# Kernel optimization log

Hardware: AMD Instinct MI355X
Metric: run time of the kernel (lower is better)

Reference implementation:

```python
import jax, jax.numpy as jnp
import numpy as np

N_NODES = 100000
N_EDGES = 1600000
N_GRAPHS = 128
IN_DIM, HID, OUT_DIM, DOC_DIM = 64, 128, 32, 768
LAYERS = 3


def setup_inputs() -> dict:
    key = jax.random.key(0)
    ks = jax.random.split(key, 24)
    s = 0.05
    inp = {
        "x": jax.random.normal(ks[0], (N_NODES, IN_DIM), jnp.float32),
        "doc_features": jax.random.normal(ks[1], (N_GRAPHS, DOC_DIM), jnp.float32),
        "edge_index": jax.random.randint(ks[2], (2, N_EDGES), 0, N_NODES, jnp.int64),
        "batch": jnp.sort(jax.random.randint(ks[3], (N_NODES,), 0, N_GRAPHS, jnp.int64)),
        # parameters (stored as [in, out] so y = x @ W + b)
        "node_w": jax.random.normal(ks[4], (IN_DIM, HID), jnp.float32) * s,
        "node_b": jnp.zeros((HID,), jnp.float32),
        "ggnn_w": jax.random.normal(ks[5], (LAYERS, HID, HID), jnp.float32) * s,
        "gru_w_ih": jax.random.normal(ks[6], (HID, 3 * HID), jnp.float32) * s,
        "gru_b_ih": jnp.zeros((3 * HID,), jnp.float32),
        "gru_w_hh": jax.random.normal(ks[7], (HID, 3 * HID), jnp.float32) * s,
        "gru_b_hh": jnp.zeros((3 * HID,), jnp.float32),
        "doc_w": jax.random.normal(ks[8], (DOC_DIM, HID), jnp.float32) * s,
        "doc_b": jnp.zeros((HID,), jnp.float32),
        "ln_g": jnp.ones((2 * HID,), jnp.float32),
        "ln_b": jnp.zeros((2 * HID,), jnp.float32),
        "fus_w": jax.random.normal(ks[9], (2 * HID, HID), jnp.float32) * s,
        "fus_b": jnp.zeros((HID,), jnp.float32),
        "task_w": jax.random.normal(ks[10], (HID, OUT_DIM), jnp.float32) * s,
        "task_b": jnp.zeros((OUT_DIM,), jnp.float32),
        "time_w": jax.random.normal(ks[11], (HID, 1), jnp.float32) * s,
        "time_b": jnp.zeros((1,), jnp.float32),
    }
    return inp


def _gru(m, h, w_ih, b_ih, w_hh, b_hh):
    gi = m @ w_ih + b_ih  # [N, 3H]
    gh = h @ w_hh + b_hh
    ir, iz, in_ = jnp.split(gi, 3, axis=-1)
    hr, hz, hn = jnp.split(gh, 3, axis=-1)
    r = jax.nn.sigmoid(ir + hr)
    z = jax.nn.sigmoid(iz + hz)
    n = jnp.tanh(in_ + r * hn)
    return (1.0 - z) * n + z * h


def reference(x, doc_features, node_w, node_b, ggnn_w, gru_w_ih, gru_b_ih,
              gru_w_hh, gru_b_hh, doc_w, doc_b, ln_g, ln_b, fus_w, fus_b,
              task_w, task_b, time_w, time_b, edge_index, batch):
    N = x.shape[0]
    src, dst = edge_index[0], edge_index[1]
    # node projection + ReLU
    h = jax.nn.relu(x @ node_w + node_b)  # [N, H]
    # GatedGraphConv: 3 layers of (linear -> scatter-add over edges -> GRU)
    for i in range(LAYERS):
        m = h @ ggnn_w[i]                              # [N, H]
        agg = jax.ops.segment_sum(m[src], dst, num_segments=N)  # scatter-add
        h = _gru(agg, h, gru_w_ih, gru_b_ih, gru_w_hh, gru_b_hh)
    # global mean pool over graphs
    sums = jax.ops.segment_sum(h, batch, num_segments=N_GRAPHS)  # [G, H]
    cnt = jax.ops.segment_sum(jnp.ones((N,), h.dtype), batch, num_segments=N_GRAPHS)
    pooled = sums / jnp.maximum(cnt, 1.0)[:, None]
    # doc projection + fusion head
    doc_emb = jax.nn.relu(doc_features @ doc_w + doc_b)  # [G, H]
    fusion = jnp.concatenate([pooled, doc_emb], axis=1)  # [G, 2H]
    mu = jnp.mean(fusion, axis=-1, keepdims=True)
    var = jnp.mean(jnp.square(fusion - mu), axis=-1, keepdims=True)
    fusion = (fusion - mu) * jax.lax.rsqrt(var + 1e-5) * ln_g + ln_b
    fusion = jax.nn.relu(fusion @ fus_w + fus_b)  # dropout is identity (eval)
    task_output = fusion @ task_w + task_b
    time_output = fusion @ time_w + time_b
    return (task_output, time_output)
```

## Files before the change

### kernel.cpp

```cpp
#include <hip/hip_runtime.h>

#define N_NODES  100000
#define N_EDGES  1600000
#define N_GRAPHS 128

#define BSH      8
#define BNODES   (1 << BSH)
#define NBUCK    391
#define NBLK_P1  512
#define EPB      (N_EDGES / NBLK_P1)
#define BKT_SCAN_N   (NBUCK * NBLK_P1)
#define SCAN_BLK_BKT 196
#define SCAN_BLK_NODE 98

typedef unsigned short u16;
typedef unsigned int   u32;
typedef __attribute__((ext_vector_type(8))) short short8;
typedef __attribute__((ext_vector_type(4))) float f32x4;

__device__ __forceinline__ float bf2f(u16 v) {
  union { u32 i; float f; } u; u.i = ((u32)v) << 16; return u.f;
}
__device__ __forceinline__ u16 f2bf(float f) {
  union { float f; u32 i; } u; u.f = f;
  u32 r = (u.i + 0x7fffu + ((u.i >> 16) & 1u)) >> 16;
  return (u16)r;
}
__device__ __forceinline__ float sigmoid_f(float x) { return 1.f / (1.f + __expf(-x)); }
__device__ __forceinline__ float tanh_f(float x) {
  x = fminf(15.f, fmaxf(-15.f, x));
  float e = __expf(2.f * x);
  return (e - 1.f) / (e + 1.f);
}
__device__ __forceinline__ int geti(const int* __restrict__ p, int i, int is64) {
  return p[is64 ? (2 * i) : i];
}

__global__ void detect_i64_kernel(const int* __restrict__ ei, const int* __restrict__ batch,
                                  int* __restrict__ flags) {
  int lane = threadIdx.x;
  {
    long long q = (long long)lane * (3200000 / 2 - 1) / 63;
    int pos = (int)(2 * q + 1);
    unsigned long long m = __ballot(ei[pos] != 0);
    if (lane == 0) flags[0] = (m == 0ull) ? 1 : 0;
  }
  {
    long long q = (long long)lane * (100000 / 2 - 1) / 63;
    int pos = (int)(2 * q + 1);
    unsigned long long m = __ballot(batch[pos] != 0);
    if (lane == 0) flags[1] = (m == 0ull) ? 1 : 0;
  }
}


__global__ __launch_bounds__(256)
void bucket_hist(const int* __restrict__ ei, const int* __restrict__ flags,
                 int* __restrict__ bcounts) {
  __shared__ int h[NBUCK];
  const int f = flags[0];
  for (int b = threadIdx.x; b < NBUCK; b += 256) h[b] = 0;
  __syncthreads();
  const int e0 = blockIdx.x * EPB;
  for (int i = threadIdx.x; i < EPB; i += 256) {
    int d = geti(ei, N_EDGES + e0 + i, f);
    atomicAdd(&h[d >> BSH], 1);
  }
  __syncthreads();
  for (int b = threadIdx.x; b < NBUCK; b += 256)
    bcounts[b * NBLK_P1 + blockIdx.x] = h[b];
}

__global__ __launch_bounds__(256)
void bucket_scatter(const int* __restrict__ ei, const int* __restrict__ flags,
                    const int* __restrict__ bbases, u32* __restrict__ bedges) {
  __shared__ int cur[NBUCK];
  const int f = flags[0];
  for (int b = threadIdx.x; b < NBUCK; b += 256)
    cur[b] = bbases[b * NBLK_P1 + blockIdx.x];
  __syncthreads();
  const int e0 = blockIdx.x * EPB;
  for (int i = threadIdx.x; i < EPB; i += 256) {
    int e = e0 + i;
    int d = geti(ei, N_EDGES + e, f);
    int s = geti(ei, e, f);
    int pos = atomicAdd(&cur[d >> BSH], 1);
    bedges[pos] = ((u32)(d & (BNODES - 1)) << 17) | (u32)s;
  }
}

__global__ __launch_bounds__(256)
void node_count(const u32* __restrict__ bedges, const int* __restrict__ bbases,
                int* __restrict__ counts) {
  __shared__ int h[BNODES];
  const int b = blockIdx.x;
  for (int i = threadIdx.x; i < BNODES; i += 256) h[i] = 0;
  __syncthreads();
  const int beg = bbases[b * NBLK_P1];
  const int end = (b + 1 < NBUCK) ? bbases[(b + 1) * NBLK_P1] : N_EDGES;
  for (int e = beg + threadIdx.x; e < end; e += 256)
    atomicAdd(&h[bedges[e] >> 17], 1);
  __syncthreads();
  const int node0 = b << BSH;
  for (int i = threadIdx.x; i < BNODES; i += 256)
    if (node0 + i < N_NODES) counts[node0 + i] = h[i];
}

__global__ __launch_bounds__(256)
void final_scatter(const u32* __restrict__ bedges, const int* __restrict__ bbases,
                   const int* __restrict__ offs, int* __restrict__ ssrc) {
  __shared__ int cur[BNODES];
  const int b = blockIdx.x;
  const int node0 = b << BSH;
  for (int i = threadIdx.x; i < BNODES; i += 256)
    cur[i] = (node0 + i < N_NODES) ? offs[node0 + i] : 0;
  __syncthreads();
  const int beg = bbases[b * NBLK_P1];
  const int end = (b + 1 < NBUCK) ? bbases[(b + 1) * NBLK_P1] : N_EDGES;
  for (int e = beg + threadIdx.x; e < end; e += 256) {
    u32 v = bedges[e];
    int pos = atomicAdd(&cur[v >> 17], 1);
    ssrc[pos] = (int)(v & 0x1FFFFu);
  }
}

__global__ __launch_bounds__(1024)
void scanA_kernel(const int* __restrict__ counts, int n, int* __restrict__ blocksums) {
  __shared__ int red[16];
  int i = blockIdx.x * 1024 + threadIdx.x;
  int v = (i < n) ? counts[i] : 0;
  for (int o = 32; o > 0; o >>= 1) v += __shfl_down(v, o, 64);
  int wv = threadIdx.x >> 6, lane = threadIdx.x & 63;
  if (lane == 0) red[wv] = v;
  __syncthreads();
  if (threadIdx.x < 16) {
    int s = red[threadIdx.x];
    for (int o = 8; o > 0; o >>= 1) s += __shfl_down(s, o, 64);
    if (threadIdx.x == 0) blocksums[blockIdx.x] = s;
  }
}

__global__ void scanB_kernel(const int* __restrict__ blocksums, int nblocks,
                             int* __restrict__ blockbase, int* __restrict__ total_out) {
  if (threadIdx.x == 0) {
    int run = 0;
    for (int b = 0; b < nblocks; ++b) { blockbase[b] = run; run += blocksums[b]; }
    if (total_out) *total_out = run;
  }
}

__global__ __launch_bounds__(1024)
void scanC_kernel(const int* __restrict__ counts, int n, const int* __restrict__ blockbase,
                  int* __restrict__ offsets) {
  __shared__ int buf[1024];
  int t = threadIdx.x;
  int i = blockIdx.x * 1024 + t;
  int v = (i < n) ? counts[i] : 0;
  buf[t] = v;
  __syncthreads();
  for (int o = 1; o < 1024; o <<= 1) {
    int add = (t >= o) ? buf[t - o] : 0;
    __syncthreads();
    buf[t] += add;
    __syncthreads();
  }
  if (i < n) offsets[i] = buf[t] - v + blockbase[blockIdx.x];
}

__global__ void transpose_kernel(const float* __restrict__ in, u16* __restrict__ out, int K, int N) {
  int i = blockIdx.x * 256 + threadIdx.x;
  if (i < K * N) {
    int k = i / N, n = i % N;
    out[n * K + k] = f2bf(in[i]);
  }
}

__global__ void wprime_kernel(const float* __restrict__ ggnn_w, const float* __restrict__ w_ih,
                              float* __restrict__ wp) {
  int i = blockIdx.x * 256 + threadIdx.x;
  if (i >= 3 * 128 * 384) return;
  int l = i / (128 * 384), r = i % (128 * 384), k = r / 384, c = r % 384;
  const float* W = ggnn_w + l * 128 * 128;
  float s = 0.f;
  for (int j = 0; j < 128; ++j) s += W[k * 128 + j] * w_ih[j * 384 + c];
  wp[i] = s;
}

__global__ void build_b2p_kernel(const float* __restrict__ wp, const float* __restrict__ w_hh,
                                 u16* __restrict__ b2p) {
  int g = blockIdx.x * 256 + threadIdx.x;
  if (g >= 8 * 1536 * 8) return;
  int e = g & 7;
  int grp = g >> 3;
  int ci = grp / 1536;
  int idx = grp % 1536;
  int n_lin = idx % 384;
  int ko = idx / 384;
  int k = ci * 32 + ko * 8 + e;
  float v = (k < 128) ? wp[k * 384 + n_lin] : w_hh[(k - 128) * 384 + n_lin];
  b2p[g] = f2bf(v);
}

__global__ __launch_bounds__(256)
void nodeproj_gemm(const float* __restrict__ A, const u16* __restrict__ BT,
                   const float* __restrict__ bias, u16* __restrict__ out, int M)
{
  constexpr int K_DIM = 64, N_DIM = 128, NT = 8, NCHUNK = 2;
  __shared__ u16 B_lds[N_DIM * 40];
  const int tid = threadIdx.x, lane = tid & 63, w = tid >> 6;
  const int strip = blockIdx.x * 64;
  const int ksub = (lane >> 4) * 8;
  union Frag { uint4 u; short8 s; };
  Frag af[NCHUNK];
  const int m_node = strip + w * 16 + (lane & 15);
  const bool avalid = (m_node < M);
#pragma unroll
  for (int ci = 0; ci < NCHUNK; ++ci) {
    int k0 = ci * 32 + ksub;
    short8 sv = {0,0,0,0,0,0,0,0};
    if (avalid) {
      const float* p = A + (size_t)m_node * K_DIM + k0;
      float4 f0 = *(const float4*)p;
      float4 f1 = *(const float4*)(p + 4);
      sv[0]=(short)f2bf(f0.x); sv[1]=(short)f2bf(f0.y); sv[2]=(short)f2bf(f0.z); sv[3]=(short)f2bf(f0.w);
      sv[4]=(short)f2bf(f1.x); sv[5]=(short)f2bf(f1.y); sv[6]=(short)f2bf(f1.z); sv[7]=(short)f2bf(f1.w);
    }
    af[ci].s = sv;
  }
  f32x4 acc[NT];
#pragma unroll
  for (int t = 0; t < NT; ++t) acc[t] = {0.f, 0.f, 0.f, 0.f};
  const int boff = (lane & 15) * 40 + ksub;
#pragma unroll
  for (int ci = 0; ci < NCHUNK; ++ci) {
    if (ci) __syncthreads();
    for (int g = tid; g < N_DIM * 4; g += 256) {
      int n = g >> 2, ko = g & 3;
      uint4 bv = *(const uint4*)(BT + (size_t)n * K_DIM + ci * 32 + ko * 8);
      *(uint4*)(&B_lds[n * 40 + ko * 8]) = bv;
    }
    __syncthreads();
    short8 a = af[ci].s;
#pragma unroll
    for (int t = 0; t < NT; ++t) {
      const short8 b = *(const short8*)(&B_lds[t * 16 * 40 + boff]);
      acc[t] = __builtin_amdgcn_mfma_f32_16x16x32_bf16(a, b, acc[t], 0, 0, 0);
    }
  }
  const int mrow = (lane >> 4) * 4;
#pragma unroll
  for (int t = 0; t < NT; ++t) {
    int col = t * 16 + (lane & 15);
    float bv = bias[col];
#pragma unroll
    for (int r = 0; r < 4; ++r) {
      int node = strip + w * 16 + mrow + r;
      if (node < M) out[(size_t)node * N_DIM + col] = f2bf(fmaxf(acc[t][r] + bv, 0.f));
    }
  }
}

__global__ __launch_bounds__(256)
void gru_gemm(const u16* __restrict__ agg, const u16* __restrict__ h,
              const u16* __restrict__ b2p, const float* __restrict__ b_ih,
              const float* __restrict__ b_hh, u16* __restrict__ hout, int M)
{
  const int tid  = threadIdx.x;
  const int lane = tid & 63;
  const int qc   = tid >> 6;
  const int strip = blockIdx.x * 32;
  const int lrow  = lane & 15;
  const int quad  = lane >> 4;
  const int ksub  = quad * 8;
  if (strip >= M) return;

  f32x4 ar[2][2], az[2][2], ain[2][2], ahn[2][2];
#pragma unroll
  for (int s = 0; s < 2; ++s)
#pragma unroll
    for (int t = 0; t < 2; ++t) {
      ar[s][t] = {0.f,0.f,0.f,0.f}; az[s][t] = {0.f,0.f,0.f,0.f};
      ain[s][t] = {0.f,0.f,0.f,0.f}; ahn[s][t] = {0.f,0.f,0.f,0.f};
    }

  union Frag { uint4 u; short8 s8; };
  const int node0 = strip + lrow;
  const int node1 = strip + 16 + lrow;
  const u16* bb = b2p + ((size_t)quad * 384 + qc * 32 + lrow) * 8;

  Frag a0[2], a1[2], fbr[2][2], fbz[2][2], fbg[2][2];

  auto ldchunk = [&](int ci, int p) {
    const u16* ap = (ci < 4) ? (agg + ci * 32 + ksub) : (h + (ci - 4) * 32 + ksub);
    a0[p].u = *(const uint4*)(ap + (size_t)node0 * 128);
    a1[p].u = *(const uint4*)(ap + (size_t)node1 * 128);
    const u16* cb = bb + ci * 12288;
    fbr[p][0].u = *(const uint4*)(cb);
    fbr[p][1].u = *(const uint4*)(cb + 128);
    fbz[p][0].u = *(const uint4*)(cb + 1024);
    fbz[p][1].u = *(const uint4*)(cb + 1024 + 128);
    fbg[p][0].u = *(const uint4*)(cb + 2048);
    fbg[p][1].u = *(const uint4*)(cb + 2048 + 128);
  };

  ldchunk(0, 0);
#pragma unroll
  for (int ci = 0; ci < 8; ++ci) {
    const int p = ci & 1, q = p ^ 1;
    if (ci < 7) ldchunk(ci + 1, q);
#pragma unroll
    for (int t = 0; t < 2; ++t) {
      ar[0][t] = __builtin_amdgcn_mfma_f32_16x16x32_bf16(a0[p].s8, fbr[p][t].s8, ar[0][t], 0, 0, 0);
      ar[1][t] = __builtin_amdgcn_mfma_f32_16x16x32_bf16(a1[p].s8, fbr[p][t].s8, ar[1][t], 0, 0, 0);
      az[0][t] = __builtin_amdgcn_mfma_f32_16x16x32_bf16(a0[p].s8, fbz[p][t].s8, az[0][t], 0, 0, 0);
      az[1][t] = __builtin_amdgcn_mfma_f32_16x16x32_bf16(a1[p].s8, fbz[p][t].s8, az[1][t], 0, 0, 0);
    }
    if (ci < 4) {
#pragma unroll
      for (int t = 0; t < 2; ++t) {
        ain[0][t] = __builtin_amdgcn_mfma_f32_16x16x32_bf16(a0[p].s8, fbg[p][t].s8, ain[0][t], 0, 0, 0);
        ain[1][t] = __builtin_amdgcn_mfma_f32_16x16x32_bf16(a1[p].s8, fbg[p][t].s8, ain[1][t], 0, 0, 0);
      }
    } else {
#pragma unroll
      for (int t = 0; t < 2; ++t) {
        ahn[0][t] = __builtin_amdgcn_mfma_f32_16x16x32_bf16(a0[p].s8, fbg[p][t].s8, ahn[0][t], 0, 0, 0);
        ahn[1][t] = __builtin_amdgcn_mfma_f32_16x16x32_bf16(a1[p].s8, fbg[p][t].s8, ahn[1][t], 0, 0, 0);
      }
    }
  }

#pragma unroll
  for (int t = 0; t < 2; ++t) {
    const int c = qc * 32 + t * 16 + lrow;
    const float brr = b_ih[c] + b_hh[c];
    const float bzz = b_ih[128 + c] + b_hh[128 + c];
    const float bin = b_ih[256 + c];
    const float bhn = b_hh[256 + c];
#pragma unroll
    for (int s = 0; s < 2; ++s) {
#pragma unroll
      for (int r = 0; r < 4; ++r) {
        const int nrow = strip + s * 16 + quad * 4 + r;
        float rg = sigmoid_f(ar[s][t][r] + brr);
        float zg = sigmoid_f(az[s][t][r] + bzz);
        float hv = ahn[s][t][r] + bhn;
        float ng = tanh_f(ain[s][t][r] + bin + rg * hv);
        float hp = bf2f(h[(size_t)nrow * 128 + c]);
        hout[(size_t)nrow * 128 + c] = f2bf((1.f - zg) * ng + zg * hp);
      }
    }
  }
}

__global__ __launch_bounds__(256)
void agg_kernel(const u16* __restrict__ m, const int* __restrict__ ssrc,
                const int* __restrict__ offsets, u16* __restrict__ agg)
{
  int node = blockIdx.x * 4 + (threadIdx.x >> 6);
  int lane = threadIdx.x & 63;
  if (node >= N_NODES) return;
  const int g = lane >> 4, l = lane & 15;
  int beg = offsets[node], end = offsets[node + 1];
  float s[8] = {0.f,0.f,0.f,0.f,0.f,0.f,0.f,0.f};
  for (int e = beg; e < end; e += 8) {
    uint4 v0 = {0u,0u,0u,0u}, v1 = {0u,0u,0u,0u};
    int e0 = e + g, e1 = e + 4 + g;
    if (e0 < end) { int src = ssrc[e0]; v0 = *(const uint4*)(m + (size_t)src * 128 + l * 8); }
    if (e1 < end) { int src = ssrc[e1]; v1 = *(const uint4*)(m + (size_t)src * 128 + l * 8); }
    u32 w0[4] = {v0.x, v0.y, v0.z, v0.w};
    u32 w1[4] = {v1.x, v1.y, v1.z, v1.w};
#pragma unroll
    for (int i = 0; i < 4; ++i) {
      s[2*i]   += bf2f((u16)(w0[i] & 0xffffu)) + bf2f((u16)(w1[i] & 0xffffu));
      s[2*i+1] += bf2f((u16)(w0[i] >> 16))     + bf2f((u16)(w1[i] >> 16));
    }
  }
#pragma unroll
  for (int i = 0; i < 8; ++i) {
    s[i] += __shfl_xor(s[i], 16, 64);
    s[i] += __shfl_xor(s[i], 32, 64);
  }
  if (g == 0) {
    uint4 o;
    o.x = (u32)f2bf(s[0]) | ((u32)f2bf(s[1]) << 16);
    o.y = (u32)f2bf(s[2]) | ((u32)f2bf(s[3]) << 16);
    o.z = (u32)f2bf(s[4]) | ((u32)f2bf(s[5]) << 16);
    o.w = (u32)f2bf(s[6]) | ((u32)f2bf(s[7]) << 16);
    *(uint4*)(agg + (size_t)node * 128 + l * 8) = o;
  }
}

__global__ __launch_bounds__(256)
void pool_kernel(const u16* __restrict__ h, const int* __restrict__ batch,
                 const int* __restrict__ flags, float* __restrict__ sums)
{
  const int c = threadIdx.x & 127;
  const int half = threadIdx.x >> 7;
  const int base = blockIdx.x * 128;
  const int f = flags[1];
  int gcur = -1; float s = 0.f;
  for (int i = half; i < 128; i += 2) {
    int n = base + i;
    if (n >= N_NODES) break;
    int g = geti(batch, n, f);
    if (g != gcur) {
      if (gcur >= 0) atomicAdd(&sums[gcur * 128 + c], s);
      s = 0.f; gcur = g;
    }
    s += bf2f(h[(size_t)n * 128 + c]);
  }
  if (gcur >= 0) atomicAdd(&sums[gcur * 128 + c], s);
}

__global__ __launch_bounds__(256)
void head2_kernel(const float* __restrict__ sums, const int* __restrict__ batch,
                  const int* __restrict__ flags,
                  const float* __restrict__ doc, const float* __restrict__ doc_w, const float* __restrict__ doc_b,
                  const float* __restrict__ ln_g, const float* __restrict__ ln_b,
                  const float* __restrict__ fus_w, const float* __restrict__ fus_b,
                  const float* __restrict__ task_w, const float* __restrict__ task_b,
                  const float* __restrict__ time_w, const float* __restrict__ time_b,
                  float* __restrict__ out_task, float* __restrict__ out_time)
{
  const int g = blockIdx.x;
  const int t = threadIdx.x;
  __shared__ float fusion[256];
  __shared__ float fh[128];
  __shared__ float dpart[256];
  __shared__ int seg[2];

  if (t < 2) {
    int f = flags[1];
    int target = g + t, lo = 0, hi = N_NODES;
    while (lo < hi) { int mid = (lo + hi) >> 1; if (geti(batch, mid, f) < target) lo = mid + 1; else hi = mid; }
    seg[t] = lo;
  }
  {
    int c = t & 127, kh = t >> 7;
    float s = 0.f;
    for (int k = kh * 384; k < kh * 384 + 384; ++k) s += doc[g * 768 + k] * doc_w[k * 128 + c];
    dpart[t] = s;
  }
  __syncthreads();

  if (t < 128) {
    float cnt = (float)(seg[1] - seg[0]);
    fusion[t] = sums[g * 128 + t] / fmaxf(cnt, 1.f);
  } else {
    int c = t - 128;
    fusion[t] = fmaxf(dpart[c] + dpart[c + 128] + doc_b[c], 0.f);
  }
  __syncthreads();

  float mu = 0.f;
  for (int i = 0; i < 256; ++i) mu += fusion[i];
  mu *= (1.f / 256.f);
  float var = 0.f;
  for (int i = 0; i < 256; ++i) { float d = fusion[i] - mu; var += d * d; }
  var *= (1.f / 256.f);
  float inv = rsqrtf(var + 1e-5f);
  float norm = (fusion[t] - mu) * inv * ln_g[t] + ln_b[t];
  __syncthreads();
  fusion[t] = norm;
  __syncthreads();

  if (t < 128) {
    float s = 0.f;
    for (int k = 0; k < 256; ++k) s += fusion[k] * fus_w[k * 128 + t];
    s += fus_b[t];
    fh[t] = fmaxf(s, 0.f);
  }
  __syncthreads();

  if (t < 32) {
    float s = 0.f;
    for (int k = 0; k < 128; ++k) s += fh[k] * task_w[k * 32 + t];
    s += task_b[t];
    out_task[g * 32 + t] = s;
  }
  if (t == 32) {
    float s = 0.f;
    for (int k = 0; k < 128; ++k) s += fh[k] * time_w[k];
    s += time_b[0];
    out_time[g] = s;
  }
}

extern "C" void kernel_launch(void* const* d_in, const int* in_sizes, int n_in,
                              void* d_out, int out_size, void* d_ws, size_t ws_size,
                              hipStream_t stream)
{
  const float* x        = (const float*)d_in[0];
  const float* doc      = (const float*)d_in[1];
  const int*   ei       = (const int*)d_in[2];
  const int*   batch    = (const int*)d_in[3];
  const float* node_w   = (const float*)d_in[4];
  const float* node_b   = (const float*)d_in[5];
  const float* ggnn_w   = (const float*)d_in[6];
  const float* gru_w_ih = (const float*)d_in[7];
  const float* gru_b_ih = (const float*)d_in[8];
  const float* gru_w_hh = (const float*)d_in[9];
  const float* gru_b_hh = (const float*)d_in[10];
  const float* doc_w    = (const float*)d_in[11];
  const float* doc_b    = (const float*)d_in[12];
  const float* ln_g     = (const float*)d_in[13];
  const float* ln_b     = (const float*)d_in[14];
  const float* fus_w    = (const float*)d_in[15];
  const float* fus_b    = (const float*)d_in[16];
  const float* task_w   = (const float*)d_in[17];
  const float* task_b   = (const float*)d_in[18];
  const float* time_w   = (const float*)d_in[19];
  const float* time_b   = (const float*)d_in[20];

  char* ws = (char*)d_ws;
  size_t off = 0;
  auto alloc = [&](size_t bytes) -> void* {
    void* p = ws + off;
    off = (off + bytes + 255) & ~(size_t)255;
    return p;
  };
  u16* aggb    = (u16*)alloc((size_t)N_NODES * 128 * 2);
  u16* hA      = (u16*)alloc((size_t)N_NODES * 128 * 2);
  u16* hB      = (u16*)alloc((size_t)N_NODES * 128 * 2);
  u16* nwT     = (u16*)alloc(64 * 128 * 2);
  u16* b2p     = (u16*)alloc(3 * 8 * 1536 * 8 * 2);
  float* wp    = (float*)alloc(3 * 128 * 384 * 4);
  float* sums  = (float*)alloc(N_GRAPHS * 128 * 4);
  int* counts  = (int*)alloc((size_t)N_NODES * 4);
  int* offs    = (int*)alloc((size_t)(N_NODES + 1) * 4);
  int* ssrc    = (int*)alloc((size_t)N_EDGES * 4);
  int* bsum    = (int*)alloc(SCAN_BLK_BKT * 4);
  int* bbase   = (int*)alloc(SCAN_BLK_BKT * 4);
  int* flags   = (int*)alloc(2 * 4);

  u32* bedges  = (u32*)aggb;
  int* bcounts = (int*)((char*)aggb + 6400000);
  int* bbases  = (int*)((char*)aggb + 7200768);

  hipMemsetAsync(sums, 0, (size_t)N_GRAPHS * 128 * 4, stream);

  detect_i64_kernel<<<1, 64, 0, stream>>>(ei, batch, flags);

  bucket_hist<<<NBLK_P1, 256, 0, stream>>>(ei, flags, bcounts);
  scanA_kernel<<<SCAN_BLK_BKT, 1024, 0, stream>>>(bcounts, BKT_SCAN_N, bsum);
  scanB_kernel<<<1, 64, 0, stream>>>(bsum, SCAN_BLK_BKT, bbase, (int*)nullptr);
  scanC_kernel<<<SCAN_BLK_BKT, 1024, 0, stream>>>(bcounts, BKT_SCAN_N, bbase, bbases);
  bucket_scatter<<<NBLK_P1, 256, 0, stream>>>(ei, flags, bbases, bedges);
  node_count<<<NBUCK, 256, 0, stream>>>(bedges, bbases, counts);
  scanA_kernel<<<SCAN_BLK_NODE, 1024, 0, stream>>>(counts, N_NODES, bsum);
  scanB_kernel<<<1, 64, 0, stream>>>(bsum, SCAN_BLK_NODE, bbase, offs + N_NODES);
  scanC_kernel<<<SCAN_BLK_NODE, 1024, 0, stream>>>(counts, N_NODES, bbase, offs);
  final_scatter<<<NBUCK, 256, 0, stream>>>(bedges, bbases, offs, ssrc);

  transpose_kernel<<<(64 * 128 + 255) / 256, 256, 0, stream>>>(node_w, nwT, 64, 128);
  wprime_kernel<<<(3 * 128 * 384 + 255) / 256, 256, 0, stream>>>(ggnn_w, gru_w_ih, wp);
  for (int l = 0; l < 3; ++l)
    build_b2p_kernel<<<(8 * 1536 * 8 + 255) / 256, 256, 0, stream>>>(
        wp + l * 128 * 384, gru_w_hh, b2p + (size_t)l * 8 * 1536 * 8);

  const int GB = (N_NODES + 63) / 64;
  const int GB32 = N_NODES / 32;
  nodeproj_gemm<<<GB, 256, 0, stream>>>(x, nwT, node_b, hA, N_NODES);

  u16* hcur = hA;
  u16* hnext = hB;
  for (int l = 0; l < 3; ++l) {
    agg_kernel<<<(N_NODES + 3) / 4, 256, 0, stream>>>(hcur, ssrc, offs, aggb);
    gru_gemm<<<GB32, 256, 0, stream>>>(aggb, hcur, b2p + (size_t)l * 8 * 1536 * 8,
                                       gru_b_ih, gru_b_hh, hnext, N_NODES);
    u16* tmp = hcur; hcur = hnext; hnext = tmp;
  }

  pool_kernel<<<(N_NODES + 127) / 128, 256, 0, stream>>>(hcur, batch, flags, sums);

  float* out_task = (float*)d_out;
  float* out_time = out_task + N_GRAPHS * 32;
  head2_kernel<<<N_GRAPHS, 256, 0, stream>>>(sums, batch, flags, doc, doc_w, doc_b, ln_g, ln_b,
                                             fus_w, fus_b, task_w, task_b, time_w, time_b,
                                             out_task, out_time);
}
```

Before: 634.6 us.

## Stage GRU weight slice in LDS and remap blocks to column quarter per 128-node strip

The GRU GEMM now assigns each block one quarter of the output columns for a 128-node strip, with each wave handling 32 nodes. The matching weight slice (48KB) is copied once into shared memory instead of every wave reloading B fragments from global memory. Activation loads are double-buffered two chunks ahead, with bounds guards for the tail. The cost is a large LDS allocation that limits occupancy, a prologue copy per block, and each A row being read by four different blocks.

Measured after the change: 669.2 us. 5.4% more time.

```diff
diff --git a/kernel.cpp b/kernel.cpp
--- a/kernel.cpp
+++ b/kernel.cpp
@@ -265,14 +265,23 @@
               const u16* __restrict__ b2p, const float* __restrict__ b_ih,
               const float* __restrict__ b_hh, u16* __restrict__ hout, int M)
 {
+  __shared__ u16 Blds[24576];
   const int tid  = threadIdx.x;
   const int lane = tid & 63;
-  const int qc   = tid >> 6;
-  const int strip = blockIdx.x * 32;
+  const int w    = tid >> 6;
+  const int qc   = blockIdx.x & 3;
+  const int strip = (blockIdx.x >> 2) * 128;
   const int lrow  = lane & 15;
   const int quad  = lane >> 4;
   const int ksub  = quad * 8;
-  if (strip >= M) return;
+
+  for (int idx = tid; idx < 3072; idx += 256) {
+    const int run = idx >> 5, off = idx & 31;
+    const int ci = run / 12, rem = run - ci * 12;
+    const int qd = rem / 3, gate = rem - qd * 3;
+    const size_t so = (size_t)ci * 12288 + qd * 3072 + gate * 1024 + qc * 256 + off * 8;
+    *(uint4*)(&Blds[run * 256 + off * 8]) = *(const uint4*)(b2p + so);
+  }
 
   f32x4 ar[2][2], az[2][2], ain[2][2], ahn[2][2];
 #pragma unroll
@@ -284,49 +293,53 @@
     }
 
   union Frag { uint4 u; short8 s8; };
-  const int node0 = strip + lrow;
-  const int node1 = strip + 16 + lrow;
-  const u16* bb = b2p + ((size_t)quad * 384 + qc * 32 + lrow) * 8;
-
-  Frag a0[2], a1[2], fbr[2][2], fbz[2][2], fbg[2][2];
-
-  auto ldchunk = [&](int ci, int p) {
+  const int node0 = strip + w * 32 + lrow;
+  const int node1 = node0 + 16;
+  const bool v0 = (node0 < M), v1 = (node1 < M);
+
+  Frag a0[2], a1[2];
+  auto lda = [&](int ci, int p) {
     const u16* ap = (ci < 4) ? (agg + ci * 32 + ksub) : (h + (ci - 4) * 32 + ksub);
-    a0[p].u = *(const uint4*)(ap + (size_t)node0 * 128);
-    a1[p].u = *(const uint4*)(ap + (size_t)node1 * 128);
-    const u16* cb = bb + ci * 12288;
-    fbr[p][0].u = *(const uint4*)(cb);
-    fbr[p][1].u = *(const uint4*)(cb + 128);
-    fbz[p][0].u = *(const uint4*)(cb + 1024);
-    fbz[p][1].u = *(const uint4*)(cb + 1024 + 128);
-    fbg[p][0].u = *(const uint4*)(cb + 2048);
-    fbg[p][1].u = *(const uint4*)(cb + 2048 + 128);
+    uint4 z = {0u,0u,0u,0u};
+    a0[p].u = v0 ? *(const uint4*)(ap + (size_t)node0 * 128) : z;
+    a1[p].u = v1 ? *(const uint4*)(ap + (size_t)node1 * 128) : z;
   };
 
-  ldchunk(0, 0);
+  lda(0, 0);
+  lda(1, 1);
+  __syncthreads();
+
 #pragma unroll
   for (int ci = 0; ci < 8; ++ci) {
-    const int p = ci & 1, q = p ^ 1;
-    if (ci < 7) ldchunk(ci + 1, q);
-#pragma unroll
-    for (int t = 0; t < 2; ++t) {
-      ar[0][t] = __builtin_amdgcn_mfma_f32_16x16x32_bf16(a0[p].s8, fbr[p][t].s8, ar[0][t], 0, 0, 0);
-      ar[1][t] = __builtin_amdgcn_mfma_f32_16x16x32_bf16(a1[p].s8, fbr[p][t].s8, ar[1][t], 0, 0, 0);
-      az[0][t] = __builtin_amdgcn_mfma_f32_16x16x32_bf16(a0[p].s8, fbz[p][t].s8, az[0][t], 0, 0, 0);
-      az[1][t] = __builtin_amdgcn_mfma_f32_16x16x32_bf16(a1[p].s8, fbz[p][t].s8, az[1][t], 0, 0, 0);
-    }
+    const int p = ci & 1;
+    const u16* lb = &Blds[ci * 3072 + quad * 768 + lrow * 8];
+    short8 br0 = *(const short8*)(lb);
+    short8 br1 = *(const short8*)(lb + 128);
+    short8 bz0 = *(const short8*)(lb + 256);
+    short8 bz1 = *(const short8*)(lb + 384);
+    short8 bg0 = *(const short8*)(lb + 512);
+    short8 bg1 = *(const short8*)(lb + 640);
+    short8 A0 = a0[p].s8, A1 = a1[p].s8;
+    if (ci < 6) lda(ci + 2, p);
+
+    ar[0][0] = __builtin_amdgcn_mfma_f32_16x16x32_bf16(A0, br0, ar[0][0], 0, 0, 0);
+    ar[1][0] = __builtin_amdgcn_mfma_f32_16x16x32_bf16(A1, br0, ar[1][0], 0, 0, 0);
+    ar[0][1] = __builtin_amdgcn_mfma_f32_16x16x32_bf16(A0, br1, ar[0][1], 0, 0, 0);
+    ar[1][1] = __builtin_amdgcn_mfma_f32_16x16x32_bf16(A1, br1, ar[1][1], 0, 0, 0);
+    az[0][0] = __builtin_amdgcn_mfma_f32_16x16x32_bf16(A0, bz0, az[0][0], 0, 0, 0);
+    az[1][0] = __builtin_amdgcn_mfma_f32_16x16x32_bf16(A1, bz0, az[1][0], 0, 0, 0);
+    az[0][1] = __builtin_amdgcn_mfma_f32_16x16x32_bf16(A0, bz1, az[0][1], 0, 0, 0);
+    az[1][1] = __builtin_amdgcn_mfma_f32_16x16x32_bf16(A1, bz1, az[1][1], 0, 0, 0);
     if (ci < 4) {
-#pragma unroll
-      for (int t = 0; t < 2; ++t) {
-        ain[0][t] = __builtin_amdgcn_mfma_f32_16x16x32_bf16(a0[p].s8, fbg[p][t].s8, ain[0][t], 0, 0, 0);
-        ain[1][t] = __builtin_amdgcn_mfma_f32_16x16x32_bf16(a1[p].s8, fbg[p][t].s8, ain[1][t], 0, 0, 0);
-      }
+      ain[0][0] = __builtin_amdgcn_mfma_f32_16x16x32_bf16(A0, bg0, ain[0][0], 0, 0, 0);
+      ain[1][0] = __builtin_amdgcn_mfma_f32_16x16x32_bf16(A1, bg0, ain[1][0], 0, 0, 0);
+      ain[0][1] = __builtin_amdgcn_mfma_f32_16x16x32_bf16(A0, bg1, ain[0][1], 0, 0, 0);
+      ain[1][1] = __builtin_amdgcn_mfma_f32_16x16x32_bf16(A1, bg1, ain[1][1], 0, 0, 0);
     } else {
-#pragma unroll
-      for (int t = 0; t < 2; ++t) {
-        ahn[0][t] = __builtin_amdgcn_mfma_f32_16x16x32_bf16(a0[p].s8, fbg[p][t].s8, ahn[0][t], 0, 0, 0);
-        ahn[1][t] = __builtin_amdgcn_mfma_f32_16x16x32_bf16(a1[p].s8, fbg[p][t].s8, ahn[1][t], 0, 0, 0);
-      }
+      ahn[0][0] = __builtin_amdgcn_mfma_f32_16x16x32_bf16(A0, bg0, ahn[0][0], 0, 0, 0);
+      ahn[1][0] = __builtin_amdgcn_mfma_f32_16x16x32_bf16(A1, bg0, ahn[1][0], 0, 0, 0);
+      ahn[0][1] = __builtin_amdgcn_mfma_f32_16x16x32_bf16(A0, bg1, ahn[0][1], 0, 0, 0);
+      ahn[1][1] = __builtin_amdgcn_mfma_f32_16x16x32_bf16(A1, bg1, ahn[1][1], 0, 0, 0);
     }
   }
 
@@ -341,13 +354,15 @@
     for (int s = 0; s < 2; ++s) {
 #pragma unroll
       for (int r = 0; r < 4; ++r) {
-        const int nrow = strip + s * 16 + quad * 4 + r;
-        float rg = sigmoid_f(ar[s][t][r] + brr);
-        float zg = sigmoid_f(az[s][t][r] + bzz);
-        float hv = ahn[s][t][r] + bhn;
-        float ng = tanh_f(ain[s][t][r] + bin + rg * hv);
-        float hp = bf2f(h[(size_t)nrow * 128 + c]);
-        hout[(size_t)nrow * 128 + c] = f2bf((1.f - zg) * ng + zg * hp);
+        const int nrow = strip + w * 32 + s * 16 + quad * 4 + r;
+        if (nrow < M) {
+          float rg = sigmoid_f(ar[s][t][r] + brr);
+          float zg = sigmoid_f(az[s][t][r] + bzz);
+          float hv = ahn[s][t][r] + bhn;
+          float ng = tanh_f(ain[s][t][r] + bin + rg * hv);
+          float hp = bf2f(h[(size_t)nrow * 128 + c]);
+          hout[(size_t)nrow * 128 + c] = f2bf((1.f - zg) * ng + zg * hp);
+        }
       }
     }
   }
@@ -560,15 +575,15 @@
         wp + l * 128 * 384, gru_w_hh, b2p + (size_t)l * 8 * 1536 * 8);
 
   const int GB = (N_NODES + 63) / 64;
-  const int GB32 = N_NODES / 32;
+  const int GBGRU = ((N_NODES + 127) / 128) * 4;
   nodeproj_gemm<<<GB, 256, 0, stream>>>(x, nwT, node_b, hA, N_NODES);
 
   u16* hcur = hA;
   u16* hnext = hB;
   for (int l = 0; l < 3; ++l) {
     agg_kernel<<<(N_NODES + 3) / 4, 256, 0, stream>>>(hcur, ssrc, offs, aggb);
-    gru_gemm<<<GB32, 256, 0, stream>>>(aggb, hcur, b2p + (size_t)l * 8 * 1536 * 8,
-                                       gru_b_ih, gru_b_hh, hnext, N_NODES);
+    gru_gemm<<<GBGRU, 256, 0, stream>>>(aggb, hcur, b2p + (size_t)l * 8 * 1536 * 8,
+                                        gru_b_ih, gru_b_hh, hnext, N_NODES);
     u16* tmp = hcur; hcur = hnext; hnext = tmp;
   }
 
```
